# Optimization experiments

Measured on AMD Instinct MI355X. Metric: run time of the kernel, lower is better.

## Reference

```python
import jax, jax.numpy as jnp
import numpy as np

NX = 8        # state dim
NU = 8        # control dim (== NX, required by original Fx assignment)
N = 64        # horizon
BATCH = 2048
M = N * NU    # condensed QP size = 512
MAX_ITER = 100
STEP = 0.01
U_MIN, U_MAX = -1.0, 1.0


def _build_buffers():
    rng = np.random.default_rng(0)
    A = rng.standard_normal((NX, NX))
    A /= 1.05 * np.max(np.abs(np.linalg.eigvals(A)))  # stable dynamics
    Bm = 0.1 * rng.standard_normal((NX, NU))
    Q = np.eye(NX)
    R = 0.1 * np.eye(NU)
    Qf = np.eye(NX)
    # Phi[k] = A^k
    Phi = np.zeros((N + 1, NX, NX))
    Phi[0] = np.eye(NX)
    for i in range(N):
        Phi[i + 1] = A @ Phi[i]
    # Gamma[i][:, j*NU:(j+1)*NU] = A^{i-1-j} B  (x_i = A^i x0 + Gamma_i u)
    Gamma = np.zeros((N + 1, NX, M))
    for i in range(1, N + 1):
        for j in range(i):
            Gamma[i, :, j * NU:(j + 1) * NU] = Phi[i - 1 - j] @ Bm
    # Condensed Hessian H_bar = sum_i Gamma_i^T Q Gamma_i + blockdiag(R) + reg
    H = np.zeros((M, M))
    for i in range(1, N):
        H += Gamma[i].T @ Q @ Gamma[i]
    H += Gamma[N].T @ Qf @ Gamma[N]
    H += np.kron(np.eye(N), R)
    H += 1e-6 * np.eye(M)
    return (jnp.asarray(H, jnp.float32), jnp.asarray(Phi, jnp.float32),
            jnp.asarray(Q, jnp.float32))


def setup_inputs() -> dict:
    key = jax.random.key(0)
    k1, k2 = jax.random.split(key)
    x0 = jax.random.normal(k1, (BATCH, NX), dtype=jnp.float32)
    xref = jax.random.normal(k2, (BATCH, N + 1, NX), dtype=jnp.float32)
    H, Phi, Q = _build_buffers()
    return {"x0": x0, "xref": xref, "H": H, "Phi": Phi, "Q": Q}


def reference(x0, xref, H, Phi, Q):
    # Linear term f: Fx_k = -2 * Phi[k] @ Q @ (xref_k - xref_0)   [B, N, NX]
    dx = xref[:, :N] - xref[:, :1]                       # [B, N, NX]
    Fx = -2.0 * jnp.einsum('kij,jl,bkl->bki', Phi[:N], Q, dx)
    f = Fx.reshape(xref.shape[0], M)                     # [B, M]

    # Projected gradient descent QP solve: 100 iterations of
    #   u <- clip(u - step*(H u + f), u_min, u_max)
    def step(u, _):
        grad = u @ H.T + f                               # [B, M]
        u_new = jnp.clip(u - STEP * grad, U_MIN, U_MAX)
        return u_new, None

    u0 = jnp.zeros_like(f)
    u, _ = jax.lax.scan(step, u0, None, length=MAX_ITER)
    return u  # full optimal control sequence [B, N*NU]
```

## Files before the change

### kernel.cpp

```cpp
#include <hip/hip_runtime.h>


typedef unsigned short u16t;
typedef __attribute__((ext_vector_type(8))) short short8;
typedef __attribute__((ext_vector_type(4))) float floatx4;

#define HLDS_BYTES (128 * 520 * 2)
#define UBF_BYTES  (16 * 520 * 2)
#define DYN_LDS    (HLDS_BYTES + UBF_BYTES)

__device__ __forceinline__ u16t f32_to_bf16(float x) {
    unsigned int u = __builtin_bit_cast(unsigned int, x);
    u = (u + 0x7FFFu + ((u >> 16) & 1u)) >> 16;
    return (u16t)u;
}

__global__ void convert_H_bf16(const float* __restrict__ H, u16t* __restrict__ Hb) {
    int idx = blockIdx.x * 256 + threadIdx.x;
    Hb[idx] = f32_to_bf16(H[idx]);
}

#define MFMA(a, b, c) __builtin_amdgcn_mfma_f32_16x16x32_bf16((a), (b), (c), 0, 0, 0)

__global__ __launch_bounds__(512, 2)
void pgd_kernel5(const float* __restrict__ xref,
                 const float* __restrict__ H,
                 const u16t*  __restrict__ Hb,
                 const float* __restrict__ Phi,
                 const float* __restrict__ Q,
                 float* __restrict__ out)
{
    extern __shared__ __align__(16) char smem[];
    u16t* Hlds = (u16t*)smem;
    u16t (*u_bf)[520] = (u16t(*)[520])(smem + HLDS_BYTES);

    const int tid  = threadIdx.x;
    const int lane = tid & 63;
    const int w    = tid >> 6;
    const int quad = lane >> 4;
    const int lcol = lane & 15;
    const int b0   = blockIdx.x * 16;
    const int colbase = w * 64;

    for (int e = tid; e < 8192; e += 512) {
        int r = e >> 6, c = e & 63;
        *(short8*)&Hlds[r * 520 + c * 8] =
            *(const short8*)&Hb[(long)((r >> 4) * 64 + 32 + (r & 15)) * 512 + c * 8];
    }
    {
        u16t* ub = &u_bf[0][0];
        for (int e = tid; e < 8320; e += 512) ub[e] = 0;
    }

    short8 hfragA[2][16];
    #pragma unroll
    for (int t = 0; t < 2; ++t) {
        const float* hrow = H + (long)(colbase + t * 16 + lcol) * 512;
        #pragma unroll
        for (int ks = 0; ks < 16; ++ks) {
            const float* hp = hrow + ks * 32 + quad * 8;
            short8 fr;
            #pragma unroll
            for (int j = 0; j < 8; ++j) fr[j] = (short)f32_to_bf16(hp[j]);
            hfragA[t][ks] = fr;
        }
    }
    short8 frag3[8];
    {
        const float* hrow = H + (long)(colbase + 48 + lcol) * 512;
        #pragma unroll
        for (int ks = 0; ks < 8; ++ks) {
            const float* hp = hrow + ks * 32 + quad * 8;
            short8 fr;
            #pragma unroll
            for (int j = 0; j < 8; ++j) fr[j] = (short)f32_to_bf16(hp[j]);
            frag3[ks] = fr;
        }
    }

    float f_reg[4][4], u_reg[4][4];
    #pragma unroll
    for (int T = 0; T < 4; ++T) {
        int c = colbase + T * 16 + lcol;
        int k = c >> 3, i = c & 7;
        #pragma unroll
        for (int r = 0; r < 4; ++r) {
            int m = quad * 4 + r;
            const float* xr = xref + (long)(b0 + m) * 520;
            float s = 0.f;
            #pragma unroll
            for (int j = 0; j < 8; ++j) {
                float z = 0.f;
                #pragma unroll
                for (int l = 0; l < 8; ++l) z += Q[j * 8 + l] * (xr[k * 8 + l] - xr[l]);
                s += Phi[k * 64 + i * 8 + j] * z;
            }
            f_reg[T][r] = -2.0f * s;
            u_reg[T][r] = 0.0f;
        }
    }
    __syncthreads();

    const u16t* hb3 = Hb + (long)(colbase + 48 + lcol) * 512;
    const u16t* h2  = Hlds + (w * 16 + lcol) * 520;

    short8 sb0 = *(const short8*)&hb3[8 * 32 + quad * 8];
    short8 sb1 = *(const short8*)&hb3[9 * 32 + quad * 8];

    for (int it = 0; it < 100; ++it) {
        floatx4 acc[4];
        #pragma unroll
        for (int T = 0; T < 4; ++T) acc[T] = (floatx4){0.f, 0.f, 0.f, 0.f};

        #pragma unroll
        for (int ks = 0; ks < 8; ++ks) {
            short8 a  = *(const short8*)&u_bf[lcol][ks * 32 + quad * 8];
            short8 b2 = *(const short8*)&h2[ks * 32 + quad * 8];
            acc[0] = MFMA(a, hfragA[0][ks], acc[0]);
            acc[1] = MFMA(a, hfragA[1][ks], acc[1]);
            acc[2] = MFMA(a, b2, acc[2]);
            acc[3] = MFMA(a, frag3[ks], acc[3]);
        }
        #pragma unroll
        for (int ks = 8; ks < 16; ++ks) {
            short8 a  = *(const short8*)&u_bf[lcol][ks * 32 + quad * 8];
            short8 b2 = *(const short8*)&h2[ks * 32 + quad * 8];
            short8 b3 = sb0;
            sb0 = sb1;
            sb1 = *(const short8*)&hb3[(8 + ((ks - 6) & 7)) * 32 + quad * 8];
            acc[0] = MFMA(a, hfragA[0][ks], acc[0]);
            acc[1] = MFMA(a, hfragA[1][ks], acc[1]);
            acc[2] = MFMA(a, b2, acc[2]);
            acc[3] = MFMA(a, b3, acc[3]);
        }

        #pragma unroll
        for (int T = 0; T < 4; ++T)
            #pragma unroll
            for (int r = 0; r < 4; ++r) {
                float g  = acc[T][r] + f_reg[T][r];
                float un = u_reg[T][r] - 0.01f * g;
                un = fminf(1.0f, fmaxf(-1.0f, un));
                u_reg[T][r] = un;
            }

        __syncthreads();
        #pragma unroll
        for (int T = 0; T < 4; ++T) {
            int c = colbase + T * 16 + lcol;
            #pragma unroll
            for (int r = 0; r < 4; ++r)
                u_bf[quad * 4 + r][c] = f32_to_bf16(u_reg[T][r]);
        }
        __syncthreads();
    }

    #pragma unroll
    for (int T = 0; T < 4; ++T) {
        int c = colbase + T * 16 + lcol;
        #pragma unroll
        for (int r = 0; r < 4; ++r)
            out[(long)(b0 + quad * 4 + r) * 512 + c] = u_reg[T][r];
    }
}

extern "C" void kernel_launch(void* const* d_in, const int* in_sizes, int n_in,
                              void* d_out, int out_size, void* d_ws, size_t ws_size,
                              hipStream_t stream) {
    const float* xref = (const float*)d_in[1];
    const float* H    = (const float*)d_in[2];
    const float* Phi  = (const float*)d_in[3];
    const float* Q    = (const float*)d_in[4];
    u16t* Hb = (u16t*)d_ws;

    (void)hipFuncSetAttribute((const void*)pgd_kernel5,
                              hipFuncAttributeMaxDynamicSharedMemorySize, DYN_LDS);

    convert_H_bf16<<<1024, 256, 0, stream>>>(H, Hb);
    pgd_kernel5<<<128, 512, DYN_LDS, stream>>>(xref, H, Hb, Phi, Q, (float*)d_out);
}
```

Before: 253.9 us.

## Double-buffer u in LDS with XOR swizzle to drop a barrier per iteration

Replaces the single padded u buffer with two ping-pong buffers, so each iteration writes the new u into the other buffer and needs only one __syncthreads instead of two. Both the H slice held in LDS and the u buffers switch from 520-element row padding to an XOR chunk swizzle, meant to avoid bank conflicts without padding. Register fragments of H are now loaded directly from the pre-converted bf16 buffer instead of converting fp32 in the kernel. LDS use rises to 160 KB, which may limit co-residency of blocks on a CU.

```diff
diff --git a/kernel.cpp b/kernel.cpp
--- a/kernel.cpp
+++ b/kernel.cpp
@@ -5,9 +5,7 @@
 typedef __attribute__((ext_vector_type(8))) short short8;
 typedef __attribute__((ext_vector_type(4))) float floatx4;
 
-#define HLDS_BYTES (128 * 520 * 2)
-#define UBF_BYTES  (16 * 520 * 2)
-#define DYN_LDS    (HLDS_BYTES + UBF_BYTES)
+#define DYN_LDS 163840
 
 __device__ __forceinline__ u16t f32_to_bf16(float x) {
     unsigned int u = __builtin_bit_cast(unsigned int, x);
@@ -23,59 +21,48 @@
 #define MFMA(a, b, c) __builtin_amdgcn_mfma_f32_16x16x32_bf16((a), (b), (c), 0, 0, 0)
 
 __global__ __launch_bounds__(512, 2)
-void pgd_kernel5(const float* __restrict__ xref,
-                 const float* __restrict__ H,
+void pgd_kernel7(const float* __restrict__ xref,
                  const u16t*  __restrict__ Hb,
                  const float* __restrict__ Phi,
                  const float* __restrict__ Q,
                  float* __restrict__ out)
 {
     extern __shared__ __align__(16) char smem[];
-    u16t* Hlds = (u16t*)smem;
-    u16t (*u_bf)[520] = (u16t(*)[520])(smem + HLDS_BYTES);
+    u16t* Hl  = (u16t*)smem;
+    u16t* ub0 = (u16t*)(smem + 131072);
+    u16t* ub1 = (u16t*)(smem + 131072 + 16384);
 
     const int tid  = threadIdx.x;
     const int lane = tid & 63;
     const int w    = tid >> 6;
     const int quad = lane >> 4;
     const int lcol = lane & 15;
+    const int l7   = lcol & 7;
     const int b0   = blockIdx.x * 16;
     const int colbase = w * 64;
 
     for (int e = tid; e < 8192; e += 512) {
         int r = e >> 6, c = e & 63;
-        *(short8*)&Hlds[r * 520 + c * 8] =
-            *(const short8*)&Hb[(long)((r >> 4) * 64 + 32 + (r & 15)) * 512 + c * 8];
+        int hrow = (r >> 4) * 64 + 32 + (r & 15);
+        *(short8*)&Hl[r * 512 + ((c ^ (r & 7)) * 8)] =
+            *(const short8*)&Hb[(long)hrow * 512 + c * 8];
     }
-    {
-        u16t* ub = &u_bf[0][0];
-        for (int e = tid; e < 8320; e += 512) ub[e] = 0;
-    }
+    for (int e = tid; e < 4096; e += 512) ((unsigned*)ub0)[e] = 0u;
 
     short8 hfragA[2][16];
     #pragma unroll
     for (int t = 0; t < 2; ++t) {
-        const float* hrow = H + (long)(colbase + t * 16 + lcol) * 512;
+        const u16t* hrow = Hb + (long)(colbase + t * 16 + lcol) * 512;
         #pragma unroll
-        for (int ks = 0; ks < 16; ++ks) {
-            const float* hp = hrow + ks * 32 + quad * 8;
-            short8 fr;
-            #pragma unroll
-            for (int j = 0; j < 8; ++j) fr[j] = (short)f32_to_bf16(hp[j]);
-            hfragA[t][ks] = fr;
-        }
+        for (int ks = 0; ks < 16; ++ks)
+            hfragA[t][ks] = *(const short8*)&hrow[ks * 32 + quad * 8];
     }
     short8 frag3[8];
     {
-        const float* hrow = H + (long)(colbase + 48 + lcol) * 512;
+        const u16t* hrow = Hb + (long)(colbase + 48 + lcol) * 512;
         #pragma unroll
-        for (int ks = 0; ks < 8; ++ks) {
-            const float* hp = hrow + ks * 32 + quad * 8;
-            short8 fr;
-            #pragma unroll
-            for (int j = 0; j < 8; ++j) fr[j] = (short)f32_to_bf16(hp[j]);
-            frag3[ks] = fr;
-        }
+        for (int ks = 0; ks < 8; ++ks)
+            frag3[ks] = *(const short8*)&hrow[ks * 32 + quad * 8];
     }
 
     float f_reg[4][4], u_reg[4][4];
@@ -101,11 +88,13 @@
     }
     __syncthreads();
 
+    const u16t* h2 = Hl + (w * 16 + lcol) * 512;
     const u16t* hb3 = Hb + (long)(colbase + 48 + lcol) * 512;
-    const u16t* h2  = Hlds + (w * 16 + lcol) * 520;
-
     short8 sb0 = *(const short8*)&hb3[8 * 32 + quad * 8];
     short8 sb1 = *(const short8*)&hb3[9 * 32 + quad * 8];
+
+    u16t* rb = ub0;
+    u16t* wb = ub1;
 
     for (int it = 0; it < 100; ++it) {
         floatx4 acc[4];
@@ -114,8 +103,9 @@
 
         #pragma unroll
         for (int ks = 0; ks < 8; ++ks) {
-            short8 a  = *(const short8*)&u_bf[lcol][ks * 32 + quad * 8];
-            short8 b2 = *(const short8*)&h2[ks * 32 + quad * 8];
+            const int sc = ((ks * 4 + quad) ^ l7) * 8;
+            short8 a  = *(const short8*)&rb[lcol * 512 + sc];
+            short8 b2 = *(const short8*)&h2[sc];
             acc[0] = MFMA(a, hfragA[0][ks], acc[0]);
             acc[1] = MFMA(a, hfragA[1][ks], acc[1]);
             acc[2] = MFMA(a, b2, acc[2]);
@@ -123,8 +113,9 @@
         }
         #pragma unroll
         for (int ks = 8; ks < 16; ++ks) {
-            short8 a  = *(const short8*)&u_bf[lcol][ks * 32 + quad * 8];
-            short8 b2 = *(const short8*)&h2[ks * 32 + quad * 8];
+            const int sc = ((ks * 4 + quad) ^ l7) * 8;
+            short8 a  = *(const short8*)&rb[lcol * 512 + sc];
+            short8 b2 = *(const short8*)&h2[sc];
             short8 b3 = sb0;
             sb0 = sb1;
             sb1 = *(const short8*)&hb3[(8 + ((ks - 6) & 7)) * 32 + quad * 8];
@@ -135,24 +126,20 @@
         }
 
         #pragma unroll
-        for (int T = 0; T < 4; ++T)
+        for (int T = 0; T < 4; ++T) {
             #pragma unroll
             for (int r = 0; r < 4; ++r) {
+                int m = quad * 4 + r;
                 float g  = acc[T][r] + f_reg[T][r];
                 float un = u_reg[T][r] - 0.01f * g;
                 un = fminf(1.0f, fmaxf(-1.0f, un));
                 u_reg[T][r] = un;
+                int chunk = (w * 8 + T * 2 + (lcol >> 3)) ^ (m & 7);
+                wb[m * 512 + chunk * 8 + l7] = f32_to_bf16(un);
             }
-
-        __syncthreads();
-        #pragma unroll
-        for (int T = 0; T < 4; ++T) {
-            int c = colbase + T * 16 + lcol;
-            #pragma unroll
-            for (int r = 0; r < 4; ++r)
-                u_bf[quad * 4 + r][c] = f32_to_bf16(u_reg[T][r]);
         }
         __syncthreads();
+        u16t* t = rb; rb = wb; wb = t;
     }
 
     #pragma unroll
@@ -173,9 +160,9 @@
     const float* Q    = (const float*)d_in[4];
     u16t* Hb = (u16t*)d_ws;
 
-    (void)hipFuncSetAttribute((const void*)pgd_kernel5,
+    (void)hipFuncSetAttribute((const void*)pgd_kernel7,
                               hipFuncAttributeMaxDynamicSharedMemorySize, DYN_LDS);
 
     convert_H_bf16<<<1024, 256, 0, stream>>>(H, Hb);
-    pgd_kernel5<<<128, 512, DYN_LDS, stream>>>(xref, H, Hb, Phi, Q, (float*)d_out);
+    pgd_kernel7<<<128, 512, DYN_LDS, stream>>>(xref, Hb, Phi, Q, (float*)d_out);
 }
```

Measured after the change: 446.1 us. +75.7%, slower.
